# Kernel optimization log

Measured on AMD Instinct MI355X. Metric: run time of the kernel, lower is better.

The kernel has to match this reference:

```python
import jax, jax.numpy as jnp
import numpy as np

N_E = 1024
E_DIM = 512
BETA = 0.25


def setup_inputs() -> dict:
    key = jax.random.key(0)
    k1, k2 = jax.random.split(key)
    z = jax.random.normal(k1, (16, E_DIM, 64, 64), dtype=jnp.float32)
    # nn.Embedding default init: N(0,1)
    codebook = jax.random.normal(k2, (N_E, E_DIM), dtype=jnp.float32)
    return {"z": z, "codebook": codebook}


def reference(z, codebook):
    # z: [B, C, H, W] -> [B, H, W, C]
    zp = jnp.transpose(z, (0, 2, 3, 1))
    B, H, W, C = zp.shape
    zf = zp.reshape(-1, C)  # [N, e_dim]
    d = (jnp.sum(zf * zf, axis=1, keepdims=True)
         + jnp.sum(codebook * codebook, axis=1)
         - 2.0 * zf @ codebook.T)
    idx = jnp.argmin(d, axis=1)  # [N]
    # one-hot @ codebook == gather
    z_q = codebook[idx].reshape(B, H, W, C)
    sg = jax.lax.stop_gradient
    e_latent_loss = jnp.mean((sg(z_q) - zp) ** 2)
    q_latent_loss = jnp.mean((z_q - sg(zp)) ** 2)
    codebook_loss = q_latent_loss + BETA * e_latent_loss
    # straight-through estimator
    z_q_st = zp + sg(z_q - zp)
    z_q_out = jnp.transpose(z_q_st, (0, 3, 1, 2))  # [B, C, H, W]
    indices = idx.reshape(B, 1, H, W)
    return (z_q_out, codebook_loss, indices)
```

## Files before the change

kernel.cpp:

```cpp
#include <hip/hip_runtime.h>

#define N_E    1024
#define E_DIM  512
#define BATCH  16
#define HW     4096
#define NROW   (BATCH * HW)
#define ZQ_SIZE (BATCH * E_DIM * HW)
#define LOSS_OFF ZQ_SIZE
#define IDX_OFF (ZQ_SIZE + 1)

typedef _Float16 half_t;
typedef __attribute__((ext_vector_type(2)))  __fp16   fp16x2;
typedef __attribute__((ext_vector_type(8)))  _Float16 frag8;
typedef __attribute__((ext_vector_type(16))) float    accv;

union U32H2 { fp16x2 h; uint32_t u; };
union FragU { uint32_t u[4]; frag8 f; };

static __device__ inline uint32_t pack2(float a, float b) {
    U32H2 t; t.h = __builtin_amdgcn_cvt_pkrtz(a, b); return t.u;
}

__global__ void k_prep_norms(const float* __restrict__ cb,
                             float* __restrict__ cn) {
    int lane = threadIdx.x & 63;
    int wid  = threadIdx.x >> 6;
    int j = blockIdx.x * 4 + wid;
    const float* row = cb + (size_t)j * E_DIM;
    float s = 0.f;
    #pragma unroll
    for (int k = 0; k < E_DIM; k += 64) {
        float v = row[k + lane];
        s += v * v;
    }
    #pragma unroll
    for (int m = 32; m >= 1; m >>= 1) s += __shfl_xor(s, m);
    if (lane == 0) cn[j] = s;
}

__global__ void k_transpose(const float* __restrict__ cb,
                            float* __restrict__ ct) {
    __shared__ float t[32][33];
    int tx = threadIdx.x & 31;
    int ty = threadIdx.x >> 5;
    int jt = blockIdx.x & 31;
    int ctl = blockIdx.x >> 5;
    int j0 = jt * 32, c0 = ctl * 32;
    #pragma unroll
    for (int i = 0; i < 4; i++) {
        int row = ty + i * 8;
        t[row][tx] = cb[(size_t)(j0 + row) * E_DIM + c0 + tx];
    }
    __syncthreads();
    #pragma unroll
    for (int i = 0; i < 4; i++) {
        int row = ty + i * 8;
        ct[(size_t)(c0 + row) * N_E + j0 + tx] = t[tx][row];
    }
}

#define ASTR 44
#define BSTR 40

__global__ __launch_bounds__(256, 2) void k_argmin_mfma(
        const float* __restrict__ z,
        const float* __restrict__ cb,
        const float* __restrict__ cn,
        int* __restrict__ idxout) {
    __shared__ uint32_t aP[128 * ASTR];
    __shared__ half_t   bH[128 * BSTR];
    __shared__ half_t   bL[128 * BSTR];
    __shared__ float    bwv[2][128];
    __shared__ int      bwi[2][128];

    int tid  = threadIdx.x;
    int lane = tid & 63;
    int l31  = lane & 31;
    int lh   = lane >> 5;
    int wm   = (tid >> 6) & 1;
    int wg   = tid >> 7;

    int n0  = blockIdx.x * 128;
    int b   = n0 >> 12;
    int hw0 = n0 & 4095;
    const float* zA = z + (size_t)b * E_DIM * HW + hw0 + 4 * (tid & 31);
    int a_kq = tid >> 5;
    int b_kq = tid & 7;
    int b_j0 = tid >> 3;

    if (tid < 128) {
        bwv[0][tid] = 3.4e38f; bwv[1][tid] = 3.4e38f;
        bwi[0][tid] = 0;       bwi[1][tid] = 0;
    }

    for (int jt = 0; jt < 8; jt++) {
        accv acc[2][2];
        #pragma unroll
        for (int mt = 0; mt < 2; mt++)
            #pragma unroll
            for (int nt = 0; nt < 2; nt++)
                #pragma unroll
                for (int i = 0; i < 16; i++) acc[mt][nt][i] = 0.f;

        for (int ks = 0; ks < 16; ks++) {
            int c0 = ks * 32;
            __syncthreads();
            {
                uint32_t pk[4][4];
                #pragma unroll
                for (int i = 0; i < 4; i++) {
                    int k = a_kq * 4 + i;
                    float4 v = *(const float4*)(zA + (size_t)(c0 + k) * HW);
                    uint32_t H01 = pack2(v.x, v.y);
                    uint32_t H23 = pack2(v.z, v.w);
                    U32H2 h01; h01.u = H01; U32H2 h23; h23.u = H23;
                    uint32_t L01 = pack2(v.x - (float)h01.h.x, v.y - (float)h01.h.y);
                    uint32_t L23 = pack2(v.z - (float)h23.h.x, v.w - (float)h23.h.y);
                    pk[0][i] = __builtin_amdgcn_perm(L01, H01, 0x05040100u);
                    pk[1][i] = __builtin_amdgcn_perm(L01, H01, 0x07060302u);
                    pk[2][i] = __builtin_amdgcn_perm(L23, H23, 0x05040100u);
                    pk[3][i] = __builtin_amdgcn_perm(L23, H23, 0x07060302u);
                }
                int m0 = (tid & 31) * 4;
                #pragma unroll
                for (int r = 0; r < 4; r++) {
                    uint4 w = make_uint4(pk[r][0], pk[r][1], pk[r][2], pk[r][3]);
                    *(uint4*)&aP[(m0 + r) * ASTR + a_kq * 4] = w;
                }
            }
            {
                const float* cbB = cb + (size_t)(jt * 128) * E_DIM + c0 + b_kq * 4;
                #pragma unroll
                for (int r = 0; r < 4; r++) {
                    int jl = b_j0 + 32 * r;
                    float4 v = *(const float4*)(cbB + (size_t)jl * E_DIM);
                    uint32_t H01 = pack2(v.x, v.y);
                    uint32_t H23 = pack2(v.z, v.w);
                    U32H2 h01; h01.u = H01; U32H2 h23; h23.u = H23;
                    uint32_t L01 = pack2(v.x - (float)h01.h.x, v.y - (float)h01.h.y);
                    uint32_t L23 = pack2(v.z - (float)h23.h.x, v.w - (float)h23.h.y);
                    *(uint2*)&bH[jl * BSTR + b_kq * 4] = make_uint2(H01, H23);
                    *(uint2*)&bL[jl * BSTR + b_kq * 4] = make_uint2(L01, L23);
                }
            }
            __syncthreads();

            #pragma unroll
            for (int ks2 = 0; ks2 < 2; ks2++) {
                int k0 = ks2 * 16 + lh * 8;
                frag8 ah[2], al[2];
                #pragma unroll
                for (int mt = 0; mt < 2; mt++) {
                    const uint32_t* pa = &aP[(wm * 64 + mt * 32 + l31) * ASTR + k0];
                    uint4 q0 = *(const uint4*)pa;
                    uint4 q1 = *(const uint4*)(pa + 4);
                    FragU uh, ul;
                    uh.u[0] = __builtin_amdgcn_perm(q0.y, q0.x, 0x05040100u);
                    uh.u[1] = __builtin_amdgcn_perm(q0.w, q0.z, 0x05040100u);
                    uh.u[2] = __builtin_amdgcn_perm(q1.y, q1.x, 0x05040100u);
                    uh.u[3] = __builtin_amdgcn_perm(q1.w, q1.z, 0x05040100u);
                    ul.u[0] = __builtin_amdgcn_perm(q0.y, q0.x, 0x07060302u);
                    ul.u[1] = __builtin_amdgcn_perm(q0.w, q0.z, 0x07060302u);
                    ul.u[2] = __builtin_amdgcn_perm(q1.y, q1.x, 0x07060302u);
                    ul.u[3] = __builtin_amdgcn_perm(q1.w, q1.z, 0x07060302u);
                    ah[mt] = uh.f; al[mt] = ul.f;
                }
                frag8 bh[2], bl[2];
                #pragma unroll
                for (int nt = 0; nt < 2; nt++) {
                    int n = wg * 64 + nt * 32 + l31;
                    bh[nt] = *(const frag8*)&bH[n * BSTR + k0];
                    bl[nt] = *(const frag8*)&bL[n * BSTR + k0];
                }
                #pragma unroll
                for (int mt = 0; mt < 2; mt++)
                    #pragma unroll
                    for (int nt = 0; nt < 2; nt++) {
                        acc[mt][nt] = __builtin_amdgcn_mfma_f32_32x32x16_f16(
                            ah[mt], bh[nt], acc[mt][nt], 0, 0, 0);
                        acc[mt][nt] = __builtin_amdgcn_mfma_f32_32x32x16_f16(
                            ah[mt], bl[nt], acc[mt][nt], 0, 0, 0);
                        acc[mt][nt] = __builtin_amdgcn_mfma_f32_32x32x16_f16(
                            al[mt], bh[nt], acc[mt][nt], 0, 0, 0);
                    }
            }
        }

        int jbase = jt * 128 + wg * 64;
        float cn0 = cn[jbase + l31];
        float cn1 = cn[jbase + 32 + l31];
        int j0i = jbase + l31, j1i = jbase + 32 + l31;
        #pragma unroll
        for (int mt = 0; mt < 2; mt++) {
            #pragma unroll
            for (int r = 0; r < 16; r++) {
                float d0 = cn0 - 2.f * acc[mt][0][r];
                float d1 = cn1 - 2.f * acc[mt][1][r];
                float v; int ix;
                if (d1 < d0) { v = d1; ix = j1i; } else { v = d0; ix = j0i; }
                #pragma unroll
                for (int m = 1; m <= 16; m <<= 1) {
                    float ov = __shfl_xor(v, m);
                    int   oi = __shfl_xor(ix, m);
                    if (ov < v || (ov == v && oi < ix)) { v = ov; ix = oi; }
                }
                if (l31 == r) {
                    int row = wm * 64 + mt * 32 + (r & 3) + 8 * (r >> 2) + 4 * lh;
                    if (v < bwv[wg][row] ||
                        (v == bwv[wg][row] && ix < bwi[wg][row])) {
                        bwv[wg][row] = v; bwi[wg][row] = ix;
                    }
                }
            }
        }
    }

    __syncthreads();
    if (tid < 128) {
        float v0 = bwv[0][tid], v1 = bwv[1][tid];
        int   i0 = bwi[0][tid], i1 = bwi[1][tid];
        int best = (v1 < v0 || (v1 == v0 && i1 < i0)) ? i1 : i0;
        idxout[n0 + tid] = best;
    }
}

__global__ void k_gather_loss(const float* __restrict__ z,
                              const float* __restrict__ ct,
                              const int* __restrict__ idx,
                              float* __restrict__ out,
                              float* __restrict__ pl) {
    int g = blockIdx.x * blockDim.x + threadIdx.x;
    int w4 = g & 1023;
    int bc = g >> 10;
    int c  = bc & 511;
    int b  = bc >> 9;
    int n4 = b * 1024 + w4;

    int4 iv = *(const int4*)(idx + (size_t)n4 * 4);
    const float* ctc = ct + (size_t)c * N_E;
    float4 zq;
    zq.x = ctc[iv.x]; zq.y = ctc[iv.y]; zq.z = ctc[iv.z]; zq.w = ctc[iv.w];
    float4 zv = *(const float4*)(z + (size_t)g * 4);

    float4 d;
    d.x = zq.x - zv.x; d.y = zq.y - zv.y; d.z = zq.z - zv.z; d.w = zq.w - zv.w;
    float4 o;
    o.x = zv.x + d.x; o.y = zv.y + d.y; o.z = zv.z + d.z; o.w = zv.w + d.w;
    *(float4*)(out + (size_t)g * 4) = o;

    float ls = d.x * d.x + d.y * d.y + d.z * d.z + d.w * d.w;
    #pragma unroll
    for (int m = 32; m >= 1; m >>= 1) ls += __shfl_xor(ls, m);

    __shared__ float wsum[4];
    int lane = threadIdx.x & 63, wid = threadIdx.x >> 6;
    if (lane == 0) wsum[wid] = ls;
    __syncthreads();
    if (threadIdx.x == 0)
        pl[blockIdx.x] = wsum[0] + wsum[1] + wsum[2] + wsum[3];

    if (c == 0) {
        float* ip = out + IDX_OFF + (size_t)n4 * 4;
        ip[0] = (float)iv.x; ip[1] = (float)iv.y;
        ip[2] = (float)iv.z; ip[3] = (float)iv.w;
    }
}

__global__ void k_final(const float* __restrict__ pl, float* __restrict__ out) {
    float s = 0.f;
    for (int i = threadIdx.x; i < 8192; i += 256) s += pl[i];
    #pragma unroll
    for (int m = 32; m >= 1; m >>= 1) s += __shfl_xor(s, m);
    __shared__ float wsum[4];
    int lane = threadIdx.x & 63, wid = threadIdx.x >> 6;
    if (lane == 0) wsum[wid] = s;
    __syncthreads();
    if (threadIdx.x == 0) {
        float tot = wsum[0] + wsum[1] + wsum[2] + wsum[3];
        out[LOSS_OFF] = 1.25f * tot / (float)ZQ_SIZE;
    }
}

extern "C" void kernel_launch(void* const* d_in, const int* in_sizes, int n_in,
                              void* d_out, int out_size, void* d_ws, size_t ws_size,
                              hipStream_t stream) {
    const float* z  = (const float*)d_in[0];
    const float* cb = (const float*)d_in[1];
    float* out = (float*)d_out;

    float* cn = (float*)d_ws + 16;
    float* ct = cn + 1024;
    int*   idx = (int*)(ct + 512 * 1024);
    float* pl  = (float*)(idx + 65536);

    k_prep_norms<<<256, 256, 0, stream>>>(cb, cn);
    k_transpose<<<512, 256, 0, stream>>>(cb, ct);
    k_argmin_mfma<<<NROW / 128, 256, 0, stream>>>(z, cb, cn, idx);
    k_gather_loss<<<ZQ_SIZE / 4 / 256, 256, 0, stream>>>(z, ct, idx, out, pl);
    k_final<<<1, 256, 0, stream>>>(pl, out);
}
```

Baseline: 615.0 us.

## Split codebook tiles across blocks with 64-bit atomicMin argmin and swizzled LDS

Each argmin block now handles one 128-row tile of z against a single 128-entry codebook tile, instead of looping over all eight codebook tiles, so the grid grows eightfold. Per-row minima are combined with a 64-bit atomicMin on an order-preserving key that packs the distance and the index; ties still go to the lower index. The norm and transpose prep kernels are merged into one launch, which also initialises the best-key buffer. The A tile in LDS gets an XOR swizzle to cut bank conflicts. The cost is global atomics and an 8-byte-per-row index buffer that the gather kernel reads back.

```diff
diff --git a/kernel.cpp b/kernel.cpp
--- a/kernel.cpp
+++ b/kernel.cpp
@@ -21,25 +21,10 @@
     U32H2 t; t.h = __builtin_amdgcn_cvt_pkrtz(a, b); return t.u;
 }
 
-__global__ void k_prep_norms(const float* __restrict__ cb,
-                             float* __restrict__ cn) {
-    int lane = threadIdx.x & 63;
-    int wid  = threadIdx.x >> 6;
-    int j = blockIdx.x * 4 + wid;
-    const float* row = cb + (size_t)j * E_DIM;
-    float s = 0.f;
-    #pragma unroll
-    for (int k = 0; k < E_DIM; k += 64) {
-        float v = row[k + lane];
-        s += v * v;
-    }
-    #pragma unroll
-    for (int m = 32; m >= 1; m >>= 1) s += __shfl_xor(s, m);
-    if (lane == 0) cn[j] = s;
-}
-
-__global__ void k_transpose(const float* __restrict__ cb,
-                            float* __restrict__ ct) {
+__global__ void k_prep(const float* __restrict__ cb,
+                       float* __restrict__ cn,
+                       float* __restrict__ ct,
+                       unsigned long long* __restrict__ best) {
     __shared__ float t[32][33];
     int tx = threadIdx.x & 31;
     int ty = threadIdx.x >> 5;
@@ -57,6 +42,25 @@
         int row = ty + i * 8;
         ct[(size_t)(c0 + row) * N_E + j0 + tx] = t[tx][row];
     }
+
+    if (blockIdx.x < 256) {
+        int lane = threadIdx.x & 63;
+        int wid  = threadIdx.x >> 6;
+        int j = blockIdx.x * 4 + wid;
+        const float* row = cb + (size_t)j * E_DIM;
+        float s = 0.f;
+        #pragma unroll
+        for (int k = 0; k < E_DIM; k += 64) {
+            float v = row[k + lane];
+            s += v * v;
+        }
+        #pragma unroll
+        for (int m = 32; m >= 1; m >>= 1) s += __shfl_xor(s, m);
+        if (lane == 0) cn[j] = s;
+    }
+
+    int g = blockIdx.x * 256 + threadIdx.x;
+    if (g < NROW) best[g] = 0xFFFFFFFFFFFFFFFFull;
 }
 
 #define ASTR 44
@@ -66,12 +70,10 @@
         const float* __restrict__ z,
         const float* __restrict__ cb,
         const float* __restrict__ cn,
-        int* __restrict__ idxout) {
+        unsigned long long* __restrict__ best) {
     __shared__ uint32_t aP[128 * ASTR];
     __shared__ half_t   bH[128 * BSTR];
     __shared__ half_t   bL[128 * BSTR];
-    __shared__ float    bwv[2][128];
-    __shared__ int      bwi[2][128];
 
     int tid  = threadIdx.x;
     int lane = tid & 63;
@@ -80,7 +82,9 @@
     int wm   = (tid >> 6) & 1;
     int wg   = tid >> 7;
 
-    int n0  = blockIdx.x * 128;
+    int jt    = blockIdx.x & 7;
+    int mtile = blockIdx.x >> 3;
+    int n0  = mtile * 128;
     int b   = n0 >> 12;
     int hw0 = n0 & 4095;
     const float* zA = z + (size_t)b * E_DIM * HW + hw0 + 4 * (tid & 31);
@@ -88,145 +92,136 @@
     int b_kq = tid & 7;
     int b_j0 = tid >> 3;
 
-    if (tid < 128) {
-        bwv[0][tid] = 3.4e38f; bwv[1][tid] = 3.4e38f;
-        bwi[0][tid] = 0;       bwi[1][tid] = 0;
-    }
-
-    for (int jt = 0; jt < 8; jt++) {
-        accv acc[2][2];
-        #pragma unroll
-        for (int mt = 0; mt < 2; mt++)
-            #pragma unroll
-            for (int nt = 0; nt < 2; nt++)
-                #pragma unroll
-                for (int i = 0; i < 16; i++) acc[mt][nt][i] = 0.f;
-
-        for (int ks = 0; ks < 16; ks++) {
-            int c0 = ks * 32;
-            __syncthreads();
-            {
-                uint32_t pk[4][4];
-                #pragma unroll
-                for (int i = 0; i < 4; i++) {
-                    int k = a_kq * 4 + i;
-                    float4 v = *(const float4*)(zA + (size_t)(c0 + k) * HW);
-                    uint32_t H01 = pack2(v.x, v.y);
-                    uint32_t H23 = pack2(v.z, v.w);
-                    U32H2 h01; h01.u = H01; U32H2 h23; h23.u = H23;
-                    uint32_t L01 = pack2(v.x - (float)h01.h.x, v.y - (float)h01.h.y);
-                    uint32_t L23 = pack2(v.z - (float)h23.h.x, v.w - (float)h23.h.y);
-                    pk[0][i] = __builtin_amdgcn_perm(L01, H01, 0x05040100u);
-                    pk[1][i] = __builtin_amdgcn_perm(L01, H01, 0x07060302u);
-                    pk[2][i] = __builtin_amdgcn_perm(L23, H23, 0x05040100u);
-                    pk[3][i] = __builtin_amdgcn_perm(L23, H23, 0x07060302u);
-                }
-                int m0 = (tid & 31) * 4;
-                #pragma unroll
-                for (int r = 0; r < 4; r++) {
-                    uint4 w = make_uint4(pk[r][0], pk[r][1], pk[r][2], pk[r][3]);
-                    *(uint4*)&aP[(m0 + r) * ASTR + a_kq * 4] = w;
-                }
-            }
-            {
-                const float* cbB = cb + (size_t)(jt * 128) * E_DIM + c0 + b_kq * 4;
-                #pragma unroll
-                for (int r = 0; r < 4; r++) {
-                    int jl = b_j0 + 32 * r;
-                    float4 v = *(const float4*)(cbB + (size_t)jl * E_DIM);
-                    uint32_t H01 = pack2(v.x, v.y);
-                    uint32_t H23 = pack2(v.z, v.w);
-                    U32H2 h01; h01.u = H01; U32H2 h23; h23.u = H23;
-                    uint32_t L01 = pack2(v.x - (float)h01.h.x, v.y - (float)h01.h.y);
-                    uint32_t L23 = pack2(v.z - (float)h23.h.x, v.w - (float)h23.h.y);
-                    *(uint2*)&bH[jl * BSTR + b_kq * 4] = make_uint2(H01, H23);
-                    *(uint2*)&bL[jl * BSTR + b_kq * 4] = make_uint2(L01, L23);
-                }
-            }
-            __syncthreads();
-
-            #pragma unroll
-            for (int ks2 = 0; ks2 < 2; ks2++) {
-                int k0 = ks2 * 16 + lh * 8;
-                frag8 ah[2], al[2];
-                #pragma unroll
-                for (int mt = 0; mt < 2; mt++) {
-                    const uint32_t* pa = &aP[(wm * 64 + mt * 32 + l31) * ASTR + k0];
-                    uint4 q0 = *(const uint4*)pa;
-                    uint4 q1 = *(const uint4*)(pa + 4);
-                    FragU uh, ul;
-                    uh.u[0] = __builtin_amdgcn_perm(q0.y, q0.x, 0x05040100u);
-                    uh.u[1] = __builtin_amdgcn_perm(q0.w, q0.z, 0x05040100u);
-                    uh.u[2] = __builtin_amdgcn_perm(q1.y, q1.x, 0x05040100u);
-                    uh.u[3] = __builtin_amdgcn_perm(q1.w, q1.z, 0x05040100u);
-                    ul.u[0] = __builtin_amdgcn_perm(q0.y, q0.x, 0x07060302u);
-                    ul.u[1] = __builtin_amdgcn_perm(q0.w, q0.z, 0x07060302u);
-                    ul.u[2] = __builtin_amdgcn_perm(q1.y, q1.x, 0x07060302u);
-                    ul.u[3] = __builtin_amdgcn_perm(q1.w, q1.z, 0x07060302u);
-                    ah[mt] = uh.f; al[mt] = ul.f;
-                }
-                frag8 bh[2], bl[2];
+    accv acc[2][2];
+    #pragma unroll
+    for (int mt = 0; mt < 2; mt++)
+        #pragma unroll
+        for (int nt = 0; nt < 2; nt++)
+            #pragma unroll
+            for (int i = 0; i < 16; i++) acc[mt][nt][i] = 0.f;
+
+    for (int ks = 0; ks < 16; ks++) {
+        int c0 = ks * 32;
+        __syncthreads();
+        {
+            uint32_t pk[4][4];
+            #pragma unroll
+            for (int i = 0; i < 4; i++) {
+                int k = a_kq * 4 + i;
+                float4 v = *(const float4*)(zA + (size_t)(c0 + k) * HW);
+                uint32_t H01 = pack2(v.x, v.y);
+                uint32_t H23 = pack2(v.z, v.w);
+                U32H2 h01; h01.u = H01; U32H2 h23; h23.u = H23;
+                uint32_t L01 = pack2(v.x - (float)h01.h.x, v.y - (float)h01.h.y);
+                uint32_t L23 = pack2(v.z - (float)h23.h.x, v.w - (float)h23.h.y);
+                pk[0][i] = __builtin_amdgcn_perm(L01, H01, 0x05040100u);
+                pk[1][i] = __builtin_amdgcn_perm(L01, H01, 0x07060302u);
+                pk[2][i] = __builtin_amdgcn_perm(L23, H23, 0x05040100u);
+                pk[3][i] = __builtin_amdgcn_perm(L23, H23, 0x07060302u);
+            }
+            int m0 = (tid & 31) * 4;
+            #pragma unroll
+            for (int r = 0; r < 4; r++) {
+                int row = m0 + r;
+                int qs = a_kq ^ ((row >> 3) & 7);
+                uint4 w = make_uint4(pk[r][0], pk[r][1], pk[r][2], pk[r][3]);
+                *(uint4*)&aP[row * ASTR + qs * 4] = w;
+            }
+        }
+        {
+            const float* cbB = cb + (size_t)(jt * 128) * E_DIM + c0 + b_kq * 4;
+            #pragma unroll
+            for (int r = 0; r < 4; r++) {
+                int jl = b_j0 + 32 * r;
+                float4 v = *(const float4*)(cbB + (size_t)jl * E_DIM);
+                uint32_t H01 = pack2(v.x, v.y);
+                uint32_t H23 = pack2(v.z, v.w);
+                U32H2 h01; h01.u = H01; U32H2 h23; h23.u = H23;
+                uint32_t L01 = pack2(v.x - (float)h01.h.x, v.y - (float)h01.h.y);
+                uint32_t L23 = pack2(v.z - (float)h23.h.x, v.w - (float)h23.h.y);
+                *(uint2*)&bH[jl * BSTR + b_kq * 4] = make_uint2(H01, H23);
+                *(uint2*)&bL[jl * BSTR + b_kq * 4] = make_uint2(L01, L23);
+            }
+        }
+        __syncthreads();
+
+        #pragma unroll
+        for (int ks2 = 0; ks2 < 2; ks2++) {
+            int k0 = ks2 * 16 + lh * 8;
+            int q0 = k0 >> 2;
+            frag8 ah[2], al[2];
+            #pragma unroll
+            for (int mt = 0; mt < 2; mt++) {
+                int row = wm * 64 + mt * 32 + l31;
+                int sw  = (row >> 3) & 7;
+                const uint32_t* pr = &aP[row * ASTR];
+                uint4 q0v = *(const uint4*)(pr + ((q0 ^ sw) << 2));
+                uint4 q1v = *(const uint4*)(pr + (((q0 + 1) ^ sw) << 2));
+                FragU uh, ul;
+                uh.u[0] = __builtin_amdgcn_perm(q0v.y, q0v.x, 0x05040100u);
+                uh.u[1] = __builtin_amdgcn_perm(q0v.w, q0v.z, 0x05040100u);
+                uh.u[2] = __builtin_amdgcn_perm(q1v.y, q1v.x, 0x05040100u);
+                uh.u[3] = __builtin_amdgcn_perm(q1v.w, q1v.z, 0x05040100u);
+                ul.u[0] = __builtin_amdgcn_perm(q0v.y, q0v.x, 0x07060302u);
+                ul.u[1] = __builtin_amdgcn_perm(q0v.w, q0v.z, 0x07060302u);
+                ul.u[2] = __builtin_amdgcn_perm(q1v.y, q1v.x, 0x07060302u);
+                ul.u[3] = __builtin_amdgcn_perm(q1v.w, q1v.z, 0x07060302u);
+                ah[mt] = uh.f; al[mt] = ul.f;
+            }
+            frag8 bh[2], bl[2];
+            #pragma unroll
+            for (int nt = 0; nt < 2; nt++) {
+                int n = wg * 64 + nt * 32 + l31;
+                bh[nt] = *(const frag8*)&bH[n * BSTR + k0];
+                bl[nt] = *(const frag8*)&bL[n * BSTR + k0];
+            }
+            #pragma unroll
+            for (int mt = 0; mt < 2; mt++)
                 #pragma unroll
                 for (int nt = 0; nt < 2; nt++) {
-                    int n = wg * 64 + nt * 32 + l31;
-                    bh[nt] = *(const frag8*)&bH[n * BSTR + k0];
-                    bl[nt] = *(const frag8*)&bL[n * BSTR + k0];
+                    acc[mt][nt] = __builtin_amdgcn_mfma_f32_32x32x16_f16(
+                        ah[mt], bh[nt], acc[mt][nt], 0, 0, 0);
+                    acc[mt][nt] = __builtin_amdgcn_mfma_f32_32x32x16_f16(
+                        ah[mt], bl[nt], acc[mt][nt], 0, 0, 0);
+                    acc[mt][nt] = __builtin_amdgcn_mfma_f32_32x32x16_f16(
+                        al[mt], bh[nt], acc[mt][nt], 0, 0, 0);
                 }
-                #pragma unroll
-                for (int mt = 0; mt < 2; mt++)
-                    #pragma unroll
-                    for (int nt = 0; nt < 2; nt++) {
-                        acc[mt][nt] = __builtin_amdgcn_mfma_f32_32x32x16_f16(
-                            ah[mt], bh[nt], acc[mt][nt], 0, 0, 0);
-                        acc[mt][nt] = __builtin_amdgcn_mfma_f32_32x32x16_f16(
-                            ah[mt], bl[nt], acc[mt][nt], 0, 0, 0);
-                        acc[mt][nt] = __builtin_amdgcn_mfma_f32_32x32x16_f16(
-                            al[mt], bh[nt], acc[mt][nt], 0, 0, 0);
-                    }
-            }
-        }
-
-        int jbase = jt * 128 + wg * 64;
-        float cn0 = cn[jbase + l31];
-        float cn1 = cn[jbase + 32 + l31];
-        int j0i = jbase + l31, j1i = jbase + 32 + l31;
-        #pragma unroll
-        for (int mt = 0; mt < 2; mt++) {
-            #pragma unroll
-            for (int r = 0; r < 16; r++) {
-                float d0 = cn0 - 2.f * acc[mt][0][r];
-                float d1 = cn1 - 2.f * acc[mt][1][r];
-                float v; int ix;
-                if (d1 < d0) { v = d1; ix = j1i; } else { v = d0; ix = j0i; }
-                #pragma unroll
-                for (int m = 1; m <= 16; m <<= 1) {
-                    float ov = __shfl_xor(v, m);
-                    int   oi = __shfl_xor(ix, m);
-                    if (ov < v || (ov == v && oi < ix)) { v = ov; ix = oi; }
-                }
-                if (l31 == r) {
-                    int row = wm * 64 + mt * 32 + (r & 3) + 8 * (r >> 2) + 4 * lh;
-                    if (v < bwv[wg][row] ||
-                        (v == bwv[wg][row] && ix < bwi[wg][row])) {
-                        bwv[wg][row] = v; bwi[wg][row] = ix;
-                    }
-                }
-            }
-        }
-    }
-
-    __syncthreads();
-    if (tid < 128) {
-        float v0 = bwv[0][tid], v1 = bwv[1][tid];
-        int   i0 = bwi[0][tid], i1 = bwi[1][tid];
-        int best = (v1 < v0 || (v1 == v0 && i1 < i0)) ? i1 : i0;
-        idxout[n0 + tid] = best;
+        }
+    }
+
+    int jbase = jt * 128 + wg * 64;
+    float cn0 = cn[jbase + l31];
+    float cn1 = cn[jbase + 32 + l31];
+    int j0i = jbase + l31, j1i = jbase + 32 + l31;
+    #pragma unroll
+    for (int mt = 0; mt < 2; mt++) {
+        #pragma unroll
+        for (int r = 0; r < 16; r++) {
+            float d0 = cn0 - 2.f * acc[mt][0][r];
+            float d1 = cn1 - 2.f * acc[mt][1][r];
+            float v; int ix;
+            if (d1 < d0) { v = d1; ix = j1i; } else { v = d0; ix = j0i; }
+            #pragma unroll
+            for (int m = 1; m <= 16; m <<= 1) {
+                float ov = __shfl_xor(v, m);
+                int   oi = __shfl_xor(ix, m);
+                if (ov < v || (ov == v && oi < ix)) { v = ov; ix = oi; }
+            }
+            if (l31 == r) {
+                int row = wm * 64 + mt * 32 + (r & 3) + 8 * (r >> 2) + 4 * lh;
+                uint32_t s = __float_as_uint(v);
+                uint32_t k32 = (s & 0x80000000u) ? ~s : (s | 0x80000000u);
+                unsigned long long key =
+                    ((unsigned long long)k32 << 32) | (uint32_t)ix;
+                atomicMin(&best[n0 + row], key);
+            }
+        }
     }
 }
 
 __global__ void k_gather_loss(const float* __restrict__ z,
                               const float* __restrict__ ct,
-                              const int* __restrict__ idx,
+                              const unsigned long long* __restrict__ best,
                               float* __restrict__ out,
                               float* __restrict__ pl) {
     int g = blockIdx.x * blockDim.x + threadIdx.x;
@@ -236,7 +231,12 @@
     int b  = bc >> 9;
     int n4 = b * 1024 + w4;
 
-    int4 iv = *(const int4*)(idx + (size_t)n4 * 4);
+    ulonglong2 b01 = *(const ulonglong2*)(best + (size_t)n4 * 4);
+    ulonglong2 b23 = *(const ulonglong2*)(best + (size_t)n4 * 4 + 2);
+    int4 iv;
+    iv.x = (int)(uint32_t)b01.x; iv.y = (int)(uint32_t)b01.y;
+    iv.z = (int)(uint32_t)b23.x; iv.w = (int)(uint32_t)b23.y;
+
     const float* ctc = ct + (size_t)c * N_E;
     float4 zq;
     zq.x = ctc[iv.x]; zq.y = ctc[iv.y]; zq.z = ctc[iv.z]; zq.w = ctc[iv.w];
@@ -290,12 +290,12 @@
 
     float* cn = (float*)d_ws + 16;
     float* ct = cn + 1024;
-    int*   idx = (int*)(ct + 512 * 1024);
-    float* pl  = (float*)(idx + 65536);
-
-    k_prep_norms<<<256, 256, 0, stream>>>(cb, cn);
-    k_transpose<<<512, 256, 0, stream>>>(cb, ct);
-    k_argmin_mfma<<<NROW / 128, 256, 0, stream>>>(z, cb, cn, idx);
-    k_gather_loss<<<ZQ_SIZE / 4 / 256, 256, 0, stream>>>(z, ct, idx, out, pl);
+    unsigned long long* best =
+        (unsigned long long*)(ct + 512 * 1024);
+    float* pl = (float*)(best + NROW);
+
+    k_prep<<<512, 256, 0, stream>>>(cb, cn, ct, best);
+    k_argmin_mfma<<<4096, 256, 0, stream>>>(z, cb, cn, best);
+    k_gather_loss<<<ZQ_SIZE / 4 / 256, 256, 0, stream>>>(z, ct, best, out, pl);
     k_final<<<1, 256, 0, stream>>>(pl, out);
 }
```

New measurement: 536.1 us. 1.15x faster.
